# Kernel optimization log

Hardware: AMD Instinct MI355X
Metric: run time of the kernel (lower is better)

Reference implementation:

```python
import jax, jax.numpy as jnp
import numpy as np

N, F_IN, HID, HEADS, E, G, CLS = 20000, 128, 32, 8, 320000, 64, 10


def setup_inputs() -> dict:
    key = jax.random.key(0)
    ks = jax.random.split(key, 16)
    HC = HEADS * HID
    inp = {
        'x': jax.random.normal(ks[0], (N, F_IN), jnp.float32),
        'edge_index': jax.random.randint(ks[1], (2, E), 0, N, jnp.int64),
        'batch': jnp.sort(jax.random.randint(ks[2], (N,), 0, G, jnp.int64)),
        'W1': jax.random.normal(ks[3], (F_IN, HC), jnp.float32) * 0.1,
        'att_l1': jax.random.normal(ks[4], (HEADS, HID), jnp.float32) * 0.1,
        'att_r1': jax.random.normal(ks[5], (HEADS, HID), jnp.float32) * 0.1,
        'b1': jnp.zeros((HC,), jnp.float32),
        'W2': jax.random.normal(ks[6], (HC, HC), jnp.float32) * 0.1,
        'att_l2': jax.random.normal(ks[7], (HEADS, HID), jnp.float32) * 0.1,
        'att_r2': jax.random.normal(ks[8], (HEADS, HID), jnp.float32) * 0.1,
        'b2': jnp.zeros((HC,), jnp.float32),
        'lin_W': jax.random.normal(ks[9], (HC, CLS), jnp.float32) * 0.1,
        'lin_b': jnp.zeros((CLS,), jnp.float32),
    }
    return inp


def _add_self_loops(edge_index):
    loops = jnp.arange(N, dtype=edge_index.dtype)
    return (jnp.concatenate([edge_index[0], loops]),
            jnp.concatenate([edge_index[1], loops]))


def _supergat_conv(x, edge_index, W, att_l, att_r, b):
    # SuperGATConv, attention_type='MX', eval mode (no dropout / neg sampling)
    h = (x @ W).reshape(-1, HEADS, HID)          # [N, H, C]
    src, dst = _add_self_loops(edge_index)       # j -> i
    x_j = h[src]                                 # [Etot, H, C]
    x_i = h[dst]
    logits = jnp.einsum('ehc,ehc->eh', x_i, x_j)            # dot-product part
    alpha = jnp.einsum('ehc,hc->eh', x_j, att_l) + jnp.einsum('ehc,hc->eh', x_i, att_r)
    alpha = alpha * jax.nn.sigmoid(logits)
    alpha = jax.nn.leaky_relu(alpha, 0.2)
    # segment softmax over incoming edges of each dst node
    amax = jax.ops.segment_max(alpha, dst, num_segments=N)
    ex = jnp.exp(alpha - amax[dst])
    denom = jax.ops.segment_sum(ex, dst, num_segments=N)
    attn = ex / (denom[dst] + 1e-16)             # [Etot, H]
    out = jax.ops.segment_sum(x_j * attn[..., None], dst, num_segments=N)  # [N,H,C]
    return out.reshape(-1, HEADS * HID) + b


def reference(x, edge_index, batch, W1, att_l1, att_r1, b1, W2, att_l2, att_r2, b2, lin_W, lin_b):
    h = _supergat_conv(x, edge_index, W1, att_l1, att_r1, b1)
    h = jax.nn.elu(h)
    h = _supergat_conv(h, edge_index, W2, att_l2, att_r2, b2)
    # global mean pool over graphs
    sums = jax.ops.segment_sum(h, batch, num_segments=G)
    cnts = jax.ops.segment_sum(jnp.ones((h.shape[0], 1), h.dtype), batch, num_segments=G)
    pooled = sums / jnp.maximum(cnts, 1.0)
    return pooled @ lin_W + lin_b
```

## Files before the change

### kernel.cpp

```cpp
#include <hip/hip_runtime.h>
#include <hip/hip_bf16.h>
#include <math.h>

#define NNODE 20000
#define FIN   128
#define HC    256
#define HEADS 8
#define HID   32
#define NEDGE 320000
#define ETOT  (NEDGE + NNODE)
#define NGRAPH 64
#define NCLS  10
#define MAXDEG 64

typedef __attribute__((ext_vector_type(8))) short short8v;
typedef __attribute__((ext_vector_type(8))) unsigned short ushort8v;
typedef __attribute__((ext_vector_type(4))) float float4v;

__device__ __forceinline__ ushort f2bf(float f) {
    __hip_bfloat16 b = __float2bfloat16(f);
    return *(ushort*)&b;
}
__device__ __forceinline__ float bf2f(ushort u) {
    return __uint_as_float(((unsigned)u) << 16);
}


#define ZB_DEG ((NNODE + 255) / 256)
#define ZB_BND ((NNODE + 255) / 256)

__global__ __launch_bounds__(256) void init_kernel(const float* __restrict__ W1,
                                                   const float* __restrict__ W2,
                                                   const int* __restrict__ batch,
                                                   ushort* __restrict__ W1t,
                                                   ushort* __restrict__ W2t,
                                                   int* __restrict__ deg,
                                                   int* __restrict__ gstart) {
    int b = blockIdx.x;
    if (b < 128) {
        int e = b * 256 + threadIdx.x;
        int k = e >> 8, n = e & 255;
        W1t[(long)n * FIN + k] = f2bf(W1[(long)k * 256 + n]);
    } else if (b < 384) {
        int e = (b - 128) * 256 + threadIdx.x;
        int k = e >> 8, n = e & 255;
        W2t[(long)n * HC + k] = f2bf(W2[(long)k * 256 + n]);
    } else if (b < 384 + ZB_DEG) {
        int i = (b - 384) * 256 + threadIdx.x;
        if (i < NNODE) deg[i] = 0;
    } else {
        int i = (b - 384 - ZB_DEG) * 256 + threadIdx.x;
        if (i < NNODE) {
            int bi = batch[i];
            if (i == 0) {
                for (int g = 0; g <= bi; g++) gstart[g] = 0;
            } else {
                int bp = batch[i - 1];
                for (int g = bp + 1; g <= bi; g++) gstart[g] = i;
            }
            if (i == NNODE - 1) {
                for (int g = bi + 1; g <= NGRAPH; g++) gstart[g] = NNODE;
            }
        }
    }
}


__global__ __launch_bounds__(256) void fill_slots(const int* __restrict__ ei,
                                                  int* __restrict__ deg,
                                                  int* __restrict__ esrc) {
    int e = blockIdx.x * blockDim.x + threadIdx.x;
    if (e >= ETOT) return;
    int src, dst;
    if (e < NEDGE) { src = ei[e]; dst = ei[NEDGE + e]; }
    else           { src = e - NEDGE; dst = src; }
    int slot = atomicAdd(&deg[dst], 1);
    if (slot < MAXDEG) esrc[dst * MAXDEG + slot] = src;
}


template<bool A_FP32>
__global__ __launch_bounds__(256) void gemm_mfma(const void* __restrict__ Aptr,
                                                 const ushort* __restrict__ Bt,
                                                 ushort* __restrict__ C,
                                                 const float* __restrict__ attL,
                                                 const float* __restrict__ attR,
                                                 float* __restrict__ aL,
                                                 float* __restrict__ aR,
                                                 int M, int K) {
    __shared__ __align__(16) ushort As[64][72];
    __shared__ __align__(16) ushort Bs[64][72];
    int tid = threadIdx.x;
    int rowBase = blockIdx.x * 64;
    int colBase = blockIdx.y * 64;
    int wave = tid >> 6;
    int l = tid & 63;
    int lm = l & 15;
    int quad = l >> 4;
    int r0 = (wave >> 1) * 32;
    int c0 = (wave & 1) * 32;

    float4v acc00 = {0.f, 0.f, 0.f, 0.f};
    float4v acc01 = acc00, acc10 = acc00, acc11 = acc00;

    float4  af[4];
    short8v ab[2];
    short8v bb[2];

    auto load_tile = [&](int k0) {
        if constexpr (A_FP32) {
            const float* A = (const float*)Aptr;
            #pragma unroll
            for (int q = 0; q < 4; q++) {
                int idx = tid + q * 256;
                int r   = idx >> 4;
                int kc  = (idx & 15) * 4;
                int grow = rowBase + r;
                float4 v = make_float4(0.f, 0.f, 0.f, 0.f);
                if (grow < M) v = *(const float4*)(A + (long)grow * K + k0 + kc);
                af[q] = v;
            }
        } else {
            const ushort* A = (const ushort*)Aptr;
            #pragma unroll
            for (int q = 0; q < 2; q++) {
                int ch = tid + q * 256;
                int r  = ch >> 3;
                int kc = (ch & 7) * 8;
                int grow = rowBase + r;
                short8v av = {};
                if (grow < M) av = *(const short8v*)(A + (long)grow * K + k0 + kc);
                ab[q] = av;
            }
        }
        #pragma unroll
        for (int q = 0; q < 2; q++) {
            int ch = tid + q * 256;
            int r  = ch >> 3;
            int kc = (ch & 7) * 8;
            bb[q] = *(const short8v*)(Bt + (long)(colBase + r) * K + k0 + kc);
        }
    };

    auto store_tile = [&]() {
        if constexpr (A_FP32) {
            #pragma unroll
            for (int q = 0; q < 4; q++) {
                int idx = tid + q * 256;
                int r   = idx >> 4;
                int kc  = (idx & 15) * 4;
                float4 v = af[q];
                ushort4 o = { f2bf(v.x), f2bf(v.y), f2bf(v.z), f2bf(v.w) };
                *(ushort4*)&As[r][kc] = o;
            }
        } else {
            #pragma unroll
            for (int q = 0; q < 2; q++) {
                int ch = tid + q * 256;
                int r  = ch >> 3;
                int kc = (ch & 7) * 8;
                *(short8v*)&As[r][kc] = ab[q];
            }
        }
        #pragma unroll
        for (int q = 0; q < 2; q++) {
            int ch = tid + q * 256;
            int r  = ch >> 3;
            int kc = (ch & 7) * 8;
            *(short8v*)&Bs[r][kc] = bb[q];
        }
    };

    load_tile(0);
    for (int k0 = 0; k0 < K; k0 += 64) {
        store_tile();
        __syncthreads();
        if (k0 + 64 < K) load_tile(k0 + 64);
        #pragma unroll
        for (int ks = 0; ks < 64; ks += 32) {
            int kb = ks + quad * 8;
            short8v a0 = *(const short8v*)&As[r0 + lm][kb];
            short8v a1 = *(const short8v*)&As[r0 + 16 + lm][kb];
            short8v b0 = *(const short8v*)&Bs[c0 + lm][kb];
            short8v b1 = *(const short8v*)&Bs[c0 + 16 + lm][kb];
            acc00 = __builtin_amdgcn_mfma_f32_16x16x32_bf16(a0, b0, acc00, 0, 0, 0);
            acc01 = __builtin_amdgcn_mfma_f32_16x16x32_bf16(a0, b1, acc01, 0, 0, 0);
            acc10 = __builtin_amdgcn_mfma_f32_16x16x32_bf16(a1, b0, acc10, 0, 0, 0);
            acc11 = __builtin_amdgcn_mfma_f32_16x16x32_bf16(a1, b1, acc11, 0, 0, 0);
        }
        __syncthreads();
    }

    int cb = colBase + c0;
    int hd = cb >> 5;
    float al0 = attL[cb + lm], al1 = attL[cb + 16 + lm];
    float ar0 = attR[cb + lm], ar1 = attR[cb + 16 + lm];
    #pragma unroll
    for (int mi = 0; mi < 2; mi++) {
        float4v s0 = mi ? acc10 : acc00;
        float4v s1 = mi ? acc11 : acc01;
        #pragma unroll
        for (int r = 0; r < 4; r++) {
            int row = rowBase + r0 + mi * 16 + quad * 4 + r;
            float pl = s0[r] * al0 + s1[r] * al1;
            float pr = s0[r] * ar0 + s1[r] * ar1;
            #pragma unroll
            for (int s2 = 1; s2 < 16; s2 <<= 1) {
                pl += __shfl_xor(pl, s2);
                pr += __shfl_xor(pr, s2);
            }
            if (row < M) {
                C[(long)row * 256 + cb + lm]      = f2bf(s0[r]);
                C[(long)row * 256 + cb + 16 + lm] = f2bf(s1[r]);
                if (lm == 0) {
                    aL[row * 8 + hd] = pl;
                    aR[row * 8 + hd] = pr;
                }
            }
        }
    }
}


__global__ __launch_bounds__(256) void fused_attn(const ushort* __restrict__ h,
                                                  const int* __restrict__ degv,
                                                  const int* __restrict__ esrc,
                                                  const float* __restrict__ aL,
                                                  const float* __restrict__ aR,
                                                  const float* __restrict__ bias,
                                                  ushort* __restrict__ out,
                                                  int apply_elu) {
    int wave = threadIdx.x >> 6;
    int node = blockIdx.x * 4 + wave;
    if (node >= NNODE) return;
    int l = threadIdx.x & 63;
    int slot = l >> 5;
    int lh = l & 31;
    int head = lh >> 2;

    const ushort8v* h8 = (const ushort8v*)h;
    ushort8v hiu = h8[(long)node * 32 + lh];
    float hi[8];
    #pragma unroll
    for (int c = 0; c < 8; c++) hi[c] = bf2f(hiu[c]);
    float a_ri = aR[node * 8 + head];
    int beg = node * MAXDEG;
    int deg = min(degv[node], MAXDEG);

    float lsum = 0.f;
    float acc[8] = {0.f, 0.f, 0.f, 0.f, 0.f, 0.f, 0.f, 0.f};

    int p  = slot;
    int j0 = (p     < deg) ? esrc[beg + p]     : 0;
    int j1 = (p + 2 < deg) ? esrc[beg + p + 2] : 0;
    int j2 = (p + 4 < deg) ? esrc[beg + p + 4] : 0;
    ushort8v hb0 = h8[(long)j0 * 32 + lh];
    float    ab0 = aL[j0 * 8 + head];
    ushort8v hb1 = h8[(long)j1 * 32 + lh];
    float    ab1 = aL[j1 * 8 + head];

    for (; p < deg; p += 2) {
        ushort8v hb2 = h8[(long)j2 * 32 + lh];
        float    ab2 = aL[j2 * 8 + head];
        int j3 = (p + 6 < deg) ? esrc[beg + p + 6] : 0;

        float hj[8];
        #pragma unroll
        for (int c = 0; c < 8; c++) hj[c] = bf2f(hb0[c]);
        float prod = hi[0] * hj[0];
        #pragma unroll
        for (int c = 1; c < 8; c++) prod += hi[c] * hj[c];
        prod += __shfl_xor(prod, 1);
        prod += __shfl_xor(prod, 2);
        float alpha = (ab0 + a_ri) * __builtin_amdgcn_rcpf(1.f + __expf(-prod));
        alpha = (alpha > 0.f) ? alpha : 0.2f * alpha;
        float ex = __expf(alpha);
        lsum += ex;
        #pragma unroll
        for (int c = 0; c < 8; c++) acc[c] += ex * hj[c];

        hb0 = hb1; ab0 = ab1;
        hb1 = hb2; ab1 = ab2;
        j2  = j3;
    }

    lsum += __shfl_xor(lsum, 32);
    #pragma unroll
    for (int c = 0; c < 8; c++) acc[c] += __shfl_xor(acc[c], 32);

    if (slot == 0) {
        float inv = __builtin_amdgcn_rcpf(lsum + 1e-16f);
        float4 b0 = ((const float4*)bias)[lh * 2];
        float4 b1 = ((const float4*)bias)[lh * 2 + 1];
        float bb[8] = {b0.x, b0.y, b0.z, b0.w, b1.x, b1.y, b1.z, b1.w};
        ushort8v o;
        #pragma unroll
        for (int c = 0; c < 8; c++) {
            float r = acc[c] * inv + bb[c];
            if (apply_elu) r = (r > 0.f) ? r : (__expf(r) - 1.f);
            o[c] = f2bf(r);
        }
        *(ushort8v*)(out + (long)node * 256 + lh * 8) = o;
    }
}


__global__ __launch_bounds__(1024) void pool_final(const ushort* __restrict__ h,
                                                   const int* __restrict__ gstart,
                                                   const float* __restrict__ linW,
                                                   const float* __restrict__ linb,
                                                   float* __restrict__ out) {
    int g = blockIdx.x;
    int t = threadIdx.x;

    int s = gstart[g];
    int e = gstart[g + 1];

    int r  = t >> 5;
    int ch = (t & 31) * 8;
    float acc[8] = {0.f, 0.f, 0.f, 0.f, 0.f, 0.f, 0.f, 0.f};
    for (int n = s + r; n < e; n += 32) {
        ushort8v v = *(const ushort8v*)(h + (long)n * 256 + ch);
        #pragma unroll
        for (int c = 0; c < 8; c++) acc[c] += bf2f(v[c]);
    }

    __shared__ float red[32][256];
    #pragma unroll
    for (int c = 0; c < 8; c++) red[r][ch + c] = acc[c];
    __syncthreads();

    __shared__ float pooled[256];
    if (t < 256) {
        float sum = 0.f;
        #pragma unroll
        for (int r2 = 0; r2 < 32; r2++) sum += red[r2][t];
        float cnt = fmaxf((float)(e - s), 1.f);
        pooled[t] = sum / cnt;
    }
    __syncthreads();

    if (t < NCLS) {
        float o = linb[t];
        for (int c = 0; c < HC; c++) o += pooled[c] * linW[c * NCLS + t];
        out[g * NCLS + t] = o;
    }
}


extern "C" void kernel_launch(void* const* d_in, const int* in_sizes, int n_in,
                              void* d_out, int out_size, void* d_ws, size_t ws_size,
                              hipStream_t stream) {
    const float* x     = (const float*)d_in[0];
    const int*   ei    = (const int*)d_in[1];
    const int*   batch = (const int*)d_in[2];
    const float* W1    = (const float*)d_in[3];
    const float* attL1 = (const float*)d_in[4];
    const float* attR1 = (const float*)d_in[5];
    const float* b1    = (const float*)d_in[6];
    const float* W2    = (const float*)d_in[7];
    const float* attL2 = (const float*)d_in[8];
    const float* attR2 = (const float*)d_in[9];
    const float* b2    = (const float*)d_in[10];
    const float* linW  = (const float*)d_in[11];
    const float* linb  = (const float*)d_in[12];
    float* out = (float*)d_out;

    char* w = (char*)d_ws;
    size_t o = 0;
    int* deg    = (int*)(w + o); o += (size_t)NNODE * 4;
    o = (o + 15) & ~(size_t)15;
    int* esrc   = (int*)(w + o); o += (size_t)NNODE * MAXDEG * 4;
    o = (o + 15) & ~(size_t)15;
    ushort* W1t = (ushort*)(w + o); o += (size_t)FIN * HC * 2;
    ushort* W2t = (ushort*)(w + o); o += (size_t)HC * HC * 2;
    o = (o + 15) & ~(size_t)15;
    ushort* hbA = (ushort*)(w + o); o += (size_t)NNODE * HC * 2;
    ushort* hbB = (ushort*)(w + o); o += (size_t)NNODE * HC * 2;
    o = (o + 15) & ~(size_t)15;
    float* aL   = (float*)(w + o); o += (size_t)NNODE * HEADS * 4;
    float* aR   = (float*)(w + o); o += (size_t)NNODE * HEADS * 4;
    o = (o + 15) & ~(size_t)15;
    int* gstart = (int*)(w + o); o += 80 * 4;

    init_kernel<<<384 + ZB_DEG + ZB_BND, 256, 0, stream>>>(W1, W2, batch, W1t, W2t, deg, gstart);

    int eb = (ETOT + 255) / 256;
    fill_slots<<<eb, 256, 0, stream>>>(ei, deg, esrc);

    dim3 gg((NNODE + 63) / 64, HC / 64);
    int ab = (NNODE + 3) / 4;
    gemm_mfma<true><<<gg, 256, 0, stream>>>(x, W1t, hbA, attL1, attR1, aL, aR, NNODE, FIN);
    fused_attn<<<ab, 256, 0, stream>>>(hbA, deg, esrc, aL, aR, b1, hbB, 1);
    gemm_mfma<false><<<gg, 256, 0, stream>>>(hbB, W2t, hbA, attL2, attR2, aL, aR, NNODE, HC);
    fused_attn<<<ab, 256, 0, stream>>>(hbA, deg, esrc, aL, aR, b2, hbB, 0);
    pool_final<<<NGRAPH, 1024, 0, stream>>>(hbB, gstart, linW, linb, out);
}
```

Baseline: 203.7 us.

## Fuse global mean-pool partial sums into second attention kernel via atomics

The second attention layer now reduces each block's four node outputs in shared memory, grouped by graph id, and atomically adds them into a per-graph fp32 sum buffer. The separate pool kernel that re-read the full bf16 node-feature matrix is replaced by a small final kernel that divides by node counts and applies the linear layer. This removes the write and re-read of the layer-2 output and avoids bf16 rounding before pooling. In exchange it adds atomics, a block barrier, and a psum zeroing stage in init. The change also raises launch bounds for occupancy, drops the early return (safe because NNODE is a multiple of 4), and converts hi to floats inside the dot loop.

```diff
diff --git a/kernel.cpp b/kernel.cpp
--- a/kernel.cpp
+++ b/kernel.cpp
@@ -28,6 +28,7 @@
 
 #define ZB_DEG ((NNODE + 255) / 256)
 #define ZB_BND ((NNODE + 255) / 256)
+#define ZB_PS  ((NGRAPH * HC + 255) / 256)
 
 __global__ __launch_bounds__(256) void init_kernel(const float* __restrict__ W1,
                                                    const float* __restrict__ W2,
@@ -35,7 +36,8 @@
                                                    ushort* __restrict__ W1t,
                                                    ushort* __restrict__ W2t,
                                                    int* __restrict__ deg,
-                                                   int* __restrict__ gstart) {
+                                                   int* __restrict__ gstart,
+                                                   float* __restrict__ psum) {
     int b = blockIdx.x;
     if (b < 128) {
         int e = b * 256 + threadIdx.x;
@@ -48,7 +50,7 @@
     } else if (b < 384 + ZB_DEG) {
         int i = (b - 384) * 256 + threadIdx.x;
         if (i < NNODE) deg[i] = 0;
-    } else {
+    } else if (b < 384 + ZB_DEG + ZB_BND) {
         int i = (b - 384 - ZB_DEG) * 256 + threadIdx.x;
         if (i < NNODE) {
             int bi = batch[i];
@@ -62,6 +64,9 @@
                 for (int g = bi + 1; g <= NGRAPH; g++) gstart[g] = NNODE;
             }
         }
+    } else {
+        int i = (b - 384 - ZB_DEG - ZB_BND) * 256 + threadIdx.x;
+        if (i < NGRAPH * HC) psum[i] = 0.f;
     }
 }
 
@@ -222,27 +227,30 @@
 }
 
 
-__global__ __launch_bounds__(256) void fused_attn(const ushort* __restrict__ h,
-                                                  const int* __restrict__ degv,
-                                                  const int* __restrict__ esrc,
-                                                  const float* __restrict__ aL,
-                                                  const float* __restrict__ aR,
-                                                  const float* __restrict__ bias,
-                                                  ushort* __restrict__ out,
-                                                  int apply_elu) {
+template<int FUSE_POOL>
+__global__ __launch_bounds__(256, 8) void fused_attn(const ushort* __restrict__ h,
+                                                     const int* __restrict__ degv,
+                                                     const int* __restrict__ esrc,
+                                                     const float* __restrict__ aL,
+                                                     const float* __restrict__ aR,
+                                                     const float* __restrict__ bias,
+                                                     ushort* __restrict__ out,
+                                                     float* __restrict__ psum,
+                                                     const int* __restrict__ batch,
+                                                     int apply_elu) {
+    __shared__ float sh[4][HC];
+    __shared__ int sgid[4];
     int wave = threadIdx.x >> 6;
     int node = blockIdx.x * 4 + wave;
-    if (node >= NNODE) return;
     int l = threadIdx.x & 63;
     int slot = l >> 5;
     int lh = l & 31;
     int head = lh >> 2;
 
+    if (FUSE_POOL && l == 0) sgid[wave] = batch[node];
+
     const ushort8v* h8 = (const ushort8v*)h;
     ushort8v hiu = h8[(long)node * 32 + lh];
-    float hi[8];
-    #pragma unroll
-    for (int c = 0; c < 8; c++) hi[c] = bf2f(hiu[c]);
     float a_ri = aR[node * 8 + head];
     int beg = node * MAXDEG;
     int deg = min(degv[node], MAXDEG);
@@ -265,11 +273,12 @@
         int j3 = (p + 6 < deg) ? esrc[beg + p + 6] : 0;
 
         float hj[8];
-        #pragma unroll
-        for (int c = 0; c < 8; c++) hj[c] = bf2f(hb0[c]);
-        float prod = hi[0] * hj[0];
-        #pragma unroll
-        for (int c = 1; c < 8; c++) prod += hi[c] * hj[c];
+        float prod = 0.f;
+        #pragma unroll
+        for (int c = 0; c < 8; c++) {
+            hj[c] = bf2f(hb0[c]);
+            prod = fmaf(bf2f(hiu[c]), hj[c], prod);
+        }
         prod += __shfl_xor(prod, 1);
         prod += __shfl_xor(prod, 2);
         float alpha = (ab0 + a_ri) * __builtin_amdgcn_rcpf(1.f + __expf(-prod));
@@ -293,53 +302,49 @@
         float4 b0 = ((const float4*)bias)[lh * 2];
         float4 b1 = ((const float4*)bias)[lh * 2 + 1];
         float bb[8] = {b0.x, b0.y, b0.z, b0.w, b1.x, b1.y, b1.z, b1.w};
-        ushort8v o;
-        #pragma unroll
-        for (int c = 0; c < 8; c++) {
-            float r = acc[c] * inv + bb[c];
-            if (apply_elu) r = (r > 0.f) ? r : (__expf(r) - 1.f);
-            o[c] = f2bf(r);
-        }
-        *(ushort8v*)(out + (long)node * 256 + lh * 8) = o;
-    }
-}
-
-
-__global__ __launch_bounds__(1024) void pool_final(const ushort* __restrict__ h,
-                                                   const int* __restrict__ gstart,
-                                                   const float* __restrict__ linW,
-                                                   const float* __restrict__ linb,
-                                                   float* __restrict__ out) {
+        if (FUSE_POOL) {
+            #pragma unroll
+            for (int c = 0; c < 8; c++)
+                sh[wave][lh * 8 + c] = acc[c] * inv + bb[c];
+        } else {
+            ushort8v o;
+            #pragma unroll
+            for (int c = 0; c < 8; c++) {
+                float r = acc[c] * inv + bb[c];
+                if (apply_elu) r = (r > 0.f) ? r : (__expf(r) - 1.f);
+                o[c] = f2bf(r);
+            }
+            *(ushort8v*)(out + (long)node * 256 + lh * 8) = o;
+        }
+    }
+
+    if (FUSE_POOL) {
+        __syncthreads();
+        int t = threadIdx.x;
+        float v = sh[0][t];
+        int g0 = sgid[0];
+        #pragma unroll
+        for (int w2 = 1; w2 < 4; w2++) {
+            int gw = sgid[w2];
+            if (gw == g0) v += sh[w2][t];
+            else { atomicAdd(&psum[g0 * HC + t], v); g0 = gw; v = sh[w2][t]; }
+        }
+        atomicAdd(&psum[g0 * HC + t], v);
+    }
+}
+
+
+__global__ __launch_bounds__(256) void final2(const float* __restrict__ psum,
+                                              const int* __restrict__ gstart,
+                                              const float* __restrict__ linW,
+                                              const float* __restrict__ linb,
+                                              float* __restrict__ out) {
     int g = blockIdx.x;
     int t = threadIdx.x;
-
-    int s = gstart[g];
-    int e = gstart[g + 1];
-
-    int r  = t >> 5;
-    int ch = (t & 31) * 8;
-    float acc[8] = {0.f, 0.f, 0.f, 0.f, 0.f, 0.f, 0.f, 0.f};
-    for (int n = s + r; n < e; n += 32) {
-        ushort8v v = *(const ushort8v*)(h + (long)n * 256 + ch);
-        #pragma unroll
-        for (int c = 0; c < 8; c++) acc[c] += bf2f(v[c]);
-    }
-
-    __shared__ float red[32][256];
-    #pragma unroll
-    for (int c = 0; c < 8; c++) red[r][ch + c] = acc[c];
+    __shared__ float pooled[HC];
+    float cnt = fmaxf((float)(gstart[g + 1] - gstart[g]), 1.f);
+    pooled[t] = psum[g * HC + t] / cnt;
     __syncthreads();
-
-    __shared__ float pooled[256];
-    if (t < 256) {
-        float sum = 0.f;
-        #pragma unroll
-        for (int r2 = 0; r2 < 32; r2++) sum += red[r2][t];
-        float cnt = fmaxf((float)(e - s), 1.f);
-        pooled[t] = sum / cnt;
-    }
-    __syncthreads();
-
     if (t < NCLS) {
         float o = linb[t];
         for (int c = 0; c < HC; c++) o += pooled[c] * linW[c * NCLS + t];
@@ -381,9 +386,11 @@
     float* aL   = (float*)(w + o); o += (size_t)NNODE * HEADS * 4;
     float* aR   = (float*)(w + o); o += (size_t)NNODE * HEADS * 4;
     o = (o + 15) & ~(size_t)15;
+    float* psum = (float*)(w + o); o += (size_t)NGRAPH * HC * 4;
     int* gstart = (int*)(w + o); o += 80 * 4;
 
-    init_kernel<<<384 + ZB_DEG + ZB_BND, 256, 0, stream>>>(W1, W2, batch, W1t, W2t, deg, gstart);
+    init_kernel<<<384 + ZB_DEG + ZB_BND + ZB_PS, 256, 0, stream>>>(
+        W1, W2, batch, W1t, W2t, deg, gstart, psum);
 
     int eb = (ETOT + 255) / 256;
     fill_slots<<<eb, 256, 0, stream>>>(ei, deg, esrc);
@@ -391,8 +398,8 @@
     dim3 gg((NNODE + 63) / 64, HC / 64);
     int ab = (NNODE + 3) / 4;
     gemm_mfma<true><<<gg, 256, 0, stream>>>(x, W1t, hbA, attL1, attR1, aL, aR, NNODE, FIN);
-    fused_attn<<<ab, 256, 0, stream>>>(hbA, deg, esrc, aL, aR, b1, hbB, 1);
+    fused_attn<0><<<ab, 256, 0, stream>>>(hbA, deg, esrc, aL, aR, b1, hbB, nullptr, batch, 1);
     gemm_mfma<false><<<gg, 256, 0, stream>>>(hbB, W2t, hbA, attL2, attR2, aL, aR, NNODE, HC);
-    fused_attn<<<ab, 256, 0, stream>>>(hbA, deg, esrc, aL, aR, b2, hbB, 0);
-    pool_final<<<NGRAPH, 1024, 0, stream>>>(hbB, gstart, linW, linb, out);
-}
+    fused_attn<1><<<ab, 256, 0, stream>>>(hbA, deg, esrc, aL, aR, b2, nullptr, psum, batch, 0);
+    final2<<<NGRAPH, 256, 0, stream>>>(psum, gstart, linW, linb, out);
+}
```

Result: faster. 199.4 us (-2.1%).
